# Kernel tuning notes

Measured on AMD Instinct MI355X. Metric: run time of the kernel, lower is better.

The kernel has to match this reference:

```python
import jax, jax.numpy as jnp
import numpy as np

GROUPS = 52
B, C, H, W = 16, 52, 256, 256  # c must equal groups (see t_value.view(b, c, 1, 1) in source)


def setup_inputs() -> dict:
    key = jax.random.key(0)
    ks = jax.random.split(key, 4)
    x = jax.random.normal(ks[0], (B, C, H, W), jnp.float32)
    weight = jax.random.normal(ks[1], (1, GROUPS, 1, 1), jnp.float32) * 0.1
    bias = jnp.ones((1, GROUPS, 1, 1), jnp.float32)
    one = jnp.ones((1, GROUPS, 1), jnp.float32)
    zero = jax.random.normal(ks[2], (1, GROUPS, 1), jnp.float32) * 0.1
    theta = jax.random.uniform(ks[3], (1, 2, 1, 1), jnp.float32)
    scale = jnp.ones((1,), jnp.float32)
    return dict(x=x, weight=weight, bias=bias, one=one, zero=zero, theta=theta, scale=scale)


def _prm_forward(x, weight, bias, one, zero, theta, scale):
    b, c, h, w = x.shape
    G = GROUPS
    cpg = c // G  # == 1 (required by original code)
    bg, hw = b * G, h * w

    xv = x.reshape(bg, cpg, hw)                      # [bg, cpg, hw]
    value = xv.sum(axis=1)                           # per-group channel-sum map [bg, hw]

    # adaptive max pool with indices (row-major argmax, first occurrence, same as torch)
    idx = jnp.argmax(value, axis=1)                  # [bg]
    qrow = (idx // w).astype(x.dtype)                # [bg]
    qcol = (idx % w).astype(x.dtype)                 # [bg]
    qval = jnp.take_along_axis(value, idx[:, None], axis=1)  # [bg, 1] == query_value

    # tiny per-group similarity matmuls (contraction over cpg)
    sim_max = jnp.einsum('gc,gch->gh', qval, xv)     # [bg, hw]
    gap = x.mean(axis=(2, 3)).reshape(bg, cpg)       # global avg pool per group-channel
    sim_gap = jnp.einsum('gc,gch->gh', gap, xv)      # [bg, hw]

    # positional Gaussian weighting: Normal(0, scale).log_prob(d * theta).exp()
    sigma = scale[0]
    log_norm = -jnp.log(sigma) - 0.5 * jnp.log(2.0 * jnp.pi)

    def gpdf(z):
        return jnp.exp(-0.5 * (z / sigma) ** 2 + log_norm)

    rows = jnp.arange(h, dtype=x.dtype)
    cols = jnp.arange(w, dtype=x.dtype)
    dr = jnp.abs(rows[None, :, None] - qrow[:, None, None])   # [bg, h, 1]
    dc = jnp.abs(cols[None, None, :] - qcol[:, None, None])   # [bg, 1, w]
    # mean over the 2 coordinate channels; broadcast avoids materializing [bg,2,h,w]
    dist = 0.5 * (gpdf(dr * theta[0, 0, 0, 0]) + gpdf(dc * theta[0, 1, 0, 0]))  # [bg, h, w]

    sim_max = sim_max.reshape(b, G, hw) * dist.reshape(b, G, hw)
    sim_gap = sim_gap.reshape(b, G, hw)
    sim = sim_max * zero + sim_gap * one             # [b, G, hw]

    # spatial mean/std normalization (torch .std -> ddof=1)
    ctx = sim - sim.mean(axis=2, keepdims=True)
    std = jnp.std(ctx, axis=2, keepdims=True, ddof=1) + 1e-05
    ctx = (ctx / std).reshape(b, G, h, w) * weight + bias

    # broadcast per-group gate over the group's channels, then sigmoid gate
    ctx = jnp.broadcast_to(ctx.reshape(bg, 1, h, w), (bg, cpg, h, w)).reshape(b, c, h, w)
    return x * jax.nn.sigmoid(ctx)


def reference(x, weight, bias, one, zero, theta, scale):
    return _prm_forward(x, weight, bias, one, zero, theta, scale)
```

## Files before the change

kernel.cpp:

```cpp
#include <hip/hip_runtime.h>
#include <math.h>

#define Gn 52
#define Hn 256
#define Wn 256
#define HW (Hn * Wn)
#define HW4 (HW / 4)
#define BG 832
#define TPB 1024
#define VPT 16

__global__ __launch_bounds__(TPB) void k_fused(
    const float4* __restrict__ x4,
    const float* __restrict__ weight, const float* __restrict__ bias,
    const float* __restrict__ one_,  const float* __restrict__ zero,
    const float* __restrict__ theta, const float* __restrict__ scale,
    float4* __restrict__ out4)
{
    const int bg   = blockIdx.x;
    const int g    = bg % Gn;
    const int t    = threadIdx.x;
    const int wave = t >> 6;
    const int lane = t & 63;
    const size_t base4 = (size_t)bg * HW4;
    const float4* xp = x4 + base4;

    float4 v[VPT];
    #pragma unroll
    for (int k = 0; k < VPT; ++k) v[k] = xp[t + k * TPB];

    float vmax = -INFINITY; int imax = 0; float sum = 0.f;
    #pragma unroll
    for (int k = 0; k < VPT; ++k) {
        int e = (t + k * TPB) * 4;
        float4 q = v[k];
        sum += (q.x + q.y) + (q.z + q.w);
        if (q.x > vmax) { vmax = q.x; imax = e; }
        if (q.y > vmax) { vmax = q.y; imax = e + 1; }
        if (q.z > vmax) { vmax = q.z; imax = e + 2; }
        if (q.w > vmax) { vmax = q.w; imax = e + 3; }
    }
    #pragma unroll
    for (int off = 32; off > 0; off >>= 1) {
        float ov = __shfl_down(vmax, off);
        int   oi = __shfl_down(imax, off);
        float os = __shfl_down(sum,  off);
        sum += os;
        if (ov > vmax || (ov == vmax && oi < imax)) { vmax = ov; imax = oi; }
    }
    __shared__ float rv[16];
    __shared__ int   ri[16];
    __shared__ float r1[16];
    __shared__ float r2[16];
    __shared__ float bc[6];
    if (lane == 0) { rv[wave] = vmax; ri[wave] = imax; r1[wave] = sum; }
    __syncthreads();
    if (t == 0) {
        float bv = rv[0]; int bi = ri[0]; float bs = r1[0];
        for (int i = 1; i < 16; ++i) {
            bs += r1[i];
            float ov = rv[i]; int oi = ri[i];
            if (ov > bv || (ov == bv && oi < bi)) { bv = ov; bi = oi; }
        }
        bc[0] = bv;
        bc[1] = (float)(bi >> 8);
        bc[2] = (float)(bi & 255);
        bc[3] = bs * (1.f / (float)HW);
    }
    __syncthreads();

    const float sigma   = scale[0];
    const float inv2s2  = 0.5f / (sigma * sigma);
    const float lognorm = -logf(sigma) - 0.9189385332046727f;
    const float th0 = theta[0], th1 = theta[1];
    const float qrow = bc[1], qcol = bc[2];
    const float A  = zero[g] * bc[0];
    const float Bc = one_[g] * bc[3];

    float s1 = 0.f, s2 = 0.f;
    #pragma unroll
    for (int k = 0; k < VPT; ++k) {
        int e = (t + k * TPB) * 4;
        float r = (float)(e >> 8);
        float c = (float)(e & 255);
        float zr = (r - qrow) * th0;
        float gr = __expf(lognorm - zr * zr * inv2s2);
        float4 q = v[k];
        #pragma unroll
        for (int j = 0; j < 4; ++j) {
            float vj = (j == 0) ? q.x : (j == 1) ? q.y : (j == 2) ? q.z : q.w;
            float zc = (c + (float)j - qcol) * th1;
            float gc = __expf(lognorm - zc * zc * inv2s2);
            float sim = (A * (0.5f * (gr + gc)) + Bc) * vj;
            s1 += sim;
            s2 += sim * sim;
        }
    }
    #pragma unroll
    for (int off = 32; off > 0; off >>= 1) {
        s1 += __shfl_down(s1, off);
        s2 += __shfl_down(s2, off);
    }
    if (lane == 0) { r1[wave] = s1; r2[wave] = s2; }
    __syncthreads();
    if (t == 0) {
        float S1 = 0.f, S2 = 0.f;
        for (int i = 0; i < 16; ++i) { S1 += r1[i]; S2 += r2[i]; }
        float mean = S1 * (1.f / (float)HW);
        float var  = (S2 - S1 * mean) * (1.f / (float)(HW - 1));
        var = fmaxf(var, 0.f);
        bc[4] = mean;
        bc[5] = weight[g] / (sqrtf(var) + 1e-5f);
    }
    __syncthreads();
    const float mean = bc[4], wsc = bc[5], bb = bias[g];

    #pragma unroll
    for (int k = 0; k < VPT; ++k) {
        int e = (t + k * TPB) * 4;
        float r = (float)(e >> 8);
        float c = (float)(e & 255);
        float zr = (r - qrow) * th0;
        float gr = __expf(lognorm - zr * zr * inv2s2);
        float4 q = v[k], o;
        #pragma unroll
        for (int j = 0; j < 4; ++j) {
            float vj = (j == 0) ? q.x : (j == 1) ? q.y : (j == 2) ? q.z : q.w;
            float zc = (c + (float)j - qcol) * th1;
            float gc = __expf(lognorm - zc * zc * inv2s2);
            float sim = (A * (0.5f * (gr + gc)) + Bc) * vj;
            float ctx = (sim - mean) * wsc + bb;
            float sg  = __builtin_amdgcn_rcpf(1.f + __expf(-ctx));
            float oj  = vj * sg;
            if (j == 0) o.x = oj; else if (j == 1) o.y = oj;
            else if (j == 2) o.z = oj; else o.w = oj;
        }
        out4[base4 + t + k * TPB] = o;
    }
}

extern "C" void kernel_launch(void* const* d_in, const int* in_sizes, int n_in,
                              void* d_out, int out_size, void* d_ws, size_t ws_size,
                              hipStream_t stream) {
    const float* x      = (const float*)d_in[0];
    const float* weight = (const float*)d_in[1];
    const float* bias   = (const float*)d_in[2];
    const float* one_   = (const float*)d_in[3];
    const float* zero   = (const float*)d_in[4];
    const float* theta  = (const float*)d_in[5];
    const float* scale  = (const float*)d_in[6];
    float* out = (float*)d_out;

    k_fused<<<BG, TPB, 0, stream>>>((const float4*)x, weight, bias, one_, zero,
                                    theta, scale, (float4*)out);
}
```

Baseline: 405.9 us.

## Precompute separable Gaussian row/column factors in LDS and streamline reductions

The per-element Gaussian weights are split into row and column terms. The 256 column values and 256 row values are computed once per block into shared memory, replacing two exp calls per element in each pass with one add. The final cross-wave reductions now use wave shuffles instead of a serial loop on thread 0. The argmax pass is split into two interleaved chains for more ILP, a launch-bounds occupancy hint is added, and the output uses nontemporal stores. The extra cost is more LDS use and one more barrier.

New measurement: 390.0 us. -3.9%, faster.

```diff
diff --git a/kernel.cpp b/kernel.cpp
--- a/kernel.cpp
+++ b/kernel.cpp
@@ -10,7 +10,9 @@
 #define TPB 1024
 #define VPT 16
 
-__global__ __launch_bounds__(TPB) void k_fused(
+typedef float vf4 __attribute__((ext_vector_type(4)));
+
+__global__ __launch_bounds__(TPB, 4) void k_fused(
     const float4* __restrict__ x4,
     const float* __restrict__ weight, const float* __restrict__ bias,
     const float* __restrict__ one_,  const float* __restrict__ zero,
@@ -25,21 +27,41 @@
     const size_t base4 = (size_t)bg * HW4;
     const float4* xp = x4 + base4;
 
+    __shared__ float rv[16];
+    __shared__ int   ri[16];
+    __shared__ float r1[16];
+    __shared__ float r2[16];
+    __shared__ float bc[6];
+    __shared__ float wcol[256];
+    __shared__ float urow[256];
+
     float4 v[VPT];
     #pragma unroll
     for (int k = 0; k < VPT; ++k) v[k] = xp[t + k * TPB];
 
-    float vmax = -INFINITY; int imax = 0; float sum = 0.f;
+    float vmaxA = -INFINITY, vmaxB = -INFINITY;
+    int   imaxA = 0x7fffffff, imaxB = 0x7fffffff;
+    float sumA = 0.f, sumB = 0.f;
     #pragma unroll
-    for (int k = 0; k < VPT; ++k) {
-        int e = (t + k * TPB) * 4;
-        float4 q = v[k];
-        sum += (q.x + q.y) + (q.z + q.w);
-        if (q.x > vmax) { vmax = q.x; imax = e; }
-        if (q.y > vmax) { vmax = q.y; imax = e + 1; }
-        if (q.z > vmax) { vmax = q.z; imax = e + 2; }
-        if (q.w > vmax) { vmax = q.w; imax = e + 3; }
+    for (int k = 0; k < VPT; k += 2) {
+        int e0 = (t + k * TPB) * 4;
+        float4 q0 = v[k];
+        sumA += (q0.x + q0.y) + (q0.z + q0.w);
+        if (q0.x > vmaxA) { vmaxA = q0.x; imaxA = e0; }
+        if (q0.y > vmaxA) { vmaxA = q0.y; imaxA = e0 + 1; }
+        if (q0.z > vmaxA) { vmaxA = q0.z; imaxA = e0 + 2; }
+        if (q0.w > vmaxA) { vmaxA = q0.w; imaxA = e0 + 3; }
+        int e1 = (t + (k + 1) * TPB) * 4;
+        float4 q1 = v[k + 1];
+        sumB += (q1.x + q1.y) + (q1.z + q1.w);
+        if (q1.x > vmaxB) { vmaxB = q1.x; imaxB = e1; }
+        if (q1.y > vmaxB) { vmaxB = q1.y; imaxB = e1 + 1; }
+        if (q1.z > vmaxB) { vmaxB = q1.z; imaxB = e1 + 2; }
+        if (q1.w > vmaxB) { vmaxB = q1.w; imaxB = e1 + 3; }
     }
+    float sum = sumA + sumB;
+    float vmax = vmaxA; int imax = imaxA;
+    if (vmaxB > vmax || (vmaxB == vmax && imaxB < imax)) { vmax = vmaxB; imax = imaxB; }
     #pragma unroll
     for (int off = 32; off > 0; off >>= 1) {
         float ov = __shfl_down(vmax, off);
@@ -48,53 +70,56 @@
         sum += os;
         if (ov > vmax || (ov == vmax && oi < imax)) { vmax = ov; imax = oi; }
     }
-    __shared__ float rv[16];
-    __shared__ int   ri[16];
-    __shared__ float r1[16];
-    __shared__ float r2[16];
-    __shared__ float bc[6];
     if (lane == 0) { rv[wave] = vmax; ri[wave] = imax; r1[wave] = sum; }
     __syncthreads();
-    if (t == 0) {
-        float bv = rv[0]; int bi = ri[0]; float bs = r1[0];
-        for (int i = 1; i < 16; ++i) {
-            bs += r1[i];
-            float ov = rv[i]; int oi = ri[i];
+    if (t < 64) {
+        float bv = (t < 16) ? rv[t] : -INFINITY;
+        int   bi = (t < 16) ? ri[t] : 0x7fffffff;
+        float bs = (t < 16) ? r1[t] : 0.f;
+        #pragma unroll
+        for (int off = 8; off > 0; off >>= 1) {
+            float ov = __shfl_down(bv, off);
+            int   oi = __shfl_down(bi, off);
+            float os = __shfl_down(bs, off);
+            bs += os;
             if (ov > bv || (ov == bv && oi < bi)) { bv = ov; bi = oi; }
         }
-        bc[0] = bv;
-        bc[1] = (float)(bi >> 8);
-        bc[2] = (float)(bi & 255);
-        bc[3] = bs * (1.f / (float)HW);
+        if (t == 0) {
+            bc[0] = bv;
+            bc[1] = (float)(bi >> 8);
+            bc[2] = (float)(bi & 255);
+            bc[3] = bs * (1.f / (float)HW);
+        }
     }
     __syncthreads();
 
     const float sigma   = scale[0];
     const float inv2s2  = 0.5f / (sigma * sigma);
     const float lognorm = -logf(sigma) - 0.9189385332046727f;
-    const float th0 = theta[0], th1 = theta[1];
-    const float qrow = bc[1], qcol = bc[2];
-    const float A  = zero[g] * bc[0];
-    const float Bc = one_[g] * bc[3];
+    const float A   = zero[g] * bc[0];
+    const float Bc  = one_[g] * bc[3];
+    const float A05 = 0.5f * A;
+    if (t < 256) {
+        float zc = ((float)t - bc[2]) * theta[1];
+        wcol[t] = A05 * __expf(lognorm - zc * zc * inv2s2);
+    } else if (t < 512) {
+        float zr = ((float)(t - 256) - bc[1]) * theta[0];
+        urow[t - 256] = A05 * __expf(lognorm - zr * zr * inv2s2) + Bc;
+    }
+    __syncthreads();
+
+    const float4 cw = *reinterpret_cast<const float4*>(&wcol[(t & 63) << 2]);
 
     float s1 = 0.f, s2 = 0.f;
     #pragma unroll
     for (int k = 0; k < VPT; ++k) {
-        int e = (t + k * TPB) * 4;
-        float r = (float)(e >> 8);
-        float c = (float)(e & 255);
-        float zr = (r - qrow) * th0;
-        float gr = __expf(lognorm - zr * zr * inv2s2);
+        const float ur = urow[wave + 16 * k];
         float4 q = v[k];
-        #pragma unroll
-        for (int j = 0; j < 4; ++j) {
-            float vj = (j == 0) ? q.x : (j == 1) ? q.y : (j == 2) ? q.z : q.w;
-            float zc = (c + (float)j - qcol) * th1;
-            float gc = __expf(lognorm - zc * zc * inv2s2);
-            float sim = (A * (0.5f * (gr + gc)) + Bc) * vj;
-            s1 += sim;
-            s2 += sim * sim;
-        }
+        float f, sim;
+        f = ur + cw.x; sim = f * q.x; s1 += sim; s2 = fmaf(sim, sim, s2);
+        f = ur + cw.y; sim = f * q.y; s1 += sim; s2 = fmaf(sim, sim, s2);
+        f = ur + cw.z; sim = f * q.z; s1 += sim; s2 = fmaf(sim, sim, s2);
+        f = ur + cw.w; sim = f * q.w; s1 += sim; s2 = fmaf(sim, sim, s2);
     }
     #pragma unroll
     for (int off = 32; off > 0; off >>= 1) {
@@ -103,39 +128,52 @@
     }
     if (lane == 0) { r1[wave] = s1; r2[wave] = s2; }
     __syncthreads();
-    if (t == 0) {
-        float S1 = 0.f, S2 = 0.f;
-        for (int i = 0; i < 16; ++i) { S1 += r1[i]; S2 += r2[i]; }
-        float mean = S1 * (1.f / (float)HW);
-        float var  = (S2 - S1 * mean) * (1.f / (float)(HW - 1));
-        var = fmaxf(var, 0.f);
-        bc[4] = mean;
-        bc[5] = weight[g] / (sqrtf(var) + 1e-5f);
+    if (t < 64) {
+        float S1 = (t < 16) ? r1[t] : 0.f;
+        float S2 = (t < 16) ? r2[t] : 0.f;
+        #pragma unroll
+        for (int off = 8; off > 0; off >>= 1) {
+            S1 += __shfl_down(S1, off);
+            S2 += __shfl_down(S2, off);
+        }
+        if (t == 0) {
+            float mean = S1 * (1.f / (float)HW);
+            float var  = (S2 - S1 * mean) * (1.f / (float)(HW - 1));
+            var = fmaxf(var, 0.f);
+            bc[4] = mean;
+            bc[5] = weight[g] / (sqrtf(var) + 1e-5f);
+        }
     }
     __syncthreads();
-    const float mean = bc[4], wsc = bc[5], bb = bias[g];
+    const float mean = bc[4], wsc = bc[5];
+    const float wb = fmaf(-mean, wsc, bias[g]);
 
     #pragma unroll
     for (int k = 0; k < VPT; ++k) {
-        int e = (t + k * TPB) * 4;
-        float r = (float)(e >> 8);
-        float c = (float)(e & 255);
-        float zr = (r - qrow) * th0;
-        float gr = __expf(lognorm - zr * zr * inv2s2);
-        float4 q = v[k], o;
-        #pragma unroll
-        for (int j = 0; j < 4; ++j) {
-            float vj = (j == 0) ? q.x : (j == 1) ? q.y : (j == 2) ? q.z : q.w;
-            float zc = (c + (float)j - qcol) * th1;
-            float gc = __expf(lognorm - zc * zc * inv2s2);
-            float sim = (A * (0.5f * (gr + gc)) + Bc) * vj;
-            float ctx = (sim - mean) * wsc + bb;
-            float sg  = __builtin_amdgcn_rcpf(1.f + __expf(-ctx));
-            float oj  = vj * sg;
-            if (j == 0) o.x = oj; else if (j == 1) o.y = oj;
-            else if (j == 2) o.z = oj; else o.w = oj;
+        const float ur = urow[wave + 16 * k];
+        float4 q = v[k];
+        vf4 o;
+        {
+            float f = ur + cw.x, sim = f * q.x;
+            float ctx = fmaf(sim, wsc, wb);
+            o.x = q.x * __builtin_amdgcn_rcpf(1.f + __expf(-ctx));
         }
-        out4[base4 + t + k * TPB] = o;
+        {
+            float f = ur + cw.y, sim = f * q.y;
+            float ctx = fmaf(sim, wsc, wb);
+            o.y = q.y * __builtin_amdgcn_rcpf(1.f + __expf(-ctx));
+        }
+        {
+            float f = ur + cw.z, sim = f * q.z;
+            float ctx = fmaf(sim, wsc, wb);
+            o.z = q.z * __builtin_amdgcn_rcpf(1.f + __expf(-ctx));
+        }
+        {
+            float f = ur + cw.w, sim = f * q.w;
+            float ctx = fmaf(sim, wsc, wb);
+            o.w = q.w * __builtin_amdgcn_rcpf(1.f + __expf(-ctx));
+        }
+        __builtin_nontemporal_store(o, reinterpret_cast<vf4*>(out4 + base4 + t + k * TPB));
     }
 }
 
```

## Split fused kernel into three strip-parallel passes with precomputed Gaussian tables

Applied to the files above, without the earlier changes.

Replaces the single kernel, which ran one 1024-thread block per slice and held the whole slice in registers, with three kernels that each split a slice into four strips of 256-thread blocks. Partial argmax, sum and moment statistics go through a small workspace buffer. Row and column Gaussian weights are precomputed into shared-memory tables, so the per-element exps drop to the sigmoid alone, and the output uses nontemporal stores. The aim is higher occupancy and less per-element transcendental work. In exchange x is read from global memory three times instead of once, and two extra launches are added.

New measurement: 434.3 us. 7.0% more time.

```diff
diff --git a/kernel.cpp b/kernel.cpp
--- a/kernel.cpp
+++ b/kernel.cpp
@@ -6,39 +6,41 @@
 #define Wn 256
 #define HW (Hn * Wn)
 #define HW4 (HW / 4)
-#define BG 832
-#define TPB 1024
-#define VPT 16
-
-__global__ __launch_bounds__(TPB) void k_fused(
-    const float4* __restrict__ x4,
-    const float* __restrict__ weight, const float* __restrict__ bias,
-    const float* __restrict__ one_,  const float* __restrict__ zero,
-    const float* __restrict__ theta, const float* __restrict__ scale,
-    float4* __restrict__ out4)
-{
-    const int bg   = blockIdx.x;
-    const int g    = bg % Gn;
-    const int t    = threadIdx.x;
-    const int wave = t >> 6;
-    const int lane = t & 63;
-    const size_t base4 = (size_t)bg * HW4;
-    const float4* xp = x4 + base4;
-
-    float4 v[VPT];
-    #pragma unroll
-    for (int k = 0; k < VPT; ++k) v[k] = xp[t + k * TPB];
-
-    float vmax = -INFINITY; int imax = 0; float sum = 0.f;
-    #pragma unroll
-    for (int k = 0; k < VPT; ++k) {
-        int e = (t + k * TPB) * 4;
-        float4 q = v[k];
-        sum += (q.x + q.y) + (q.z + q.w);
-        if (q.x > vmax) { vmax = q.x; imax = e; }
-        if (q.y > vmax) { vmax = q.y; imax = e + 1; }
-        if (q.z > vmax) { vmax = q.z; imax = e + 2; }
-        if (q.w > vmax) { vmax = q.w; imax = e + 3; }
+#define NSLICE 832
+#define SPB 4
+#define NBLK (NSLICE * SPB)
+#define TPB 256
+#define STRIP4 (HW4 / SPB)
+#define VPT (STRIP4 / TPB)
+#define WSS 24
+
+typedef float vf4 __attribute__((ext_vector_type(4)));
+
+__global__ __launch_bounds__(TPB) void k_p1(
+    const float4* __restrict__ x4, float* __restrict__ ws)
+{
+    const int blk = blockIdx.x;
+    const int bg = blk >> 2, q = blk & 3;
+    const int t = threadIdx.x;
+    const int wave = t >> 6, lane = t & 63;
+    const float4* xp = x4 + (size_t)bg * HW4 + q * STRIP4;
+
+    float vmax = -INFINITY; int imax = 0x7fffffff; float sum = 0.f;
+    #pragma unroll
+    for (int kk = 0; kk < VPT; kk += 4) {
+        float4 b[4];
+        #pragma unroll
+        for (int u = 0; u < 4; ++u) b[u] = xp[t + (kk + u) * TPB];
+        #pragma unroll
+        for (int u = 0; u < 4; ++u) {
+            int e = (q * STRIP4 + t + (kk + u) * TPB) * 4;
+            float4 v = b[u];
+            sum += (v.x + v.y) + (v.z + v.w);
+            if (v.x > vmax) { vmax = v.x; imax = e; }
+            if (v.y > vmax) { vmax = v.y; imax = e + 1; }
+            if (v.z > vmax) { vmax = v.z; imax = e + 2; }
+            if (v.w > vmax) { vmax = v.w; imax = e + 3; }
+        }
     }
     #pragma unroll
     for (int off = 32; off > 0; off >>= 1) {
@@ -48,52 +50,92 @@
         sum += os;
         if (ov > vmax || (ov == vmax && oi < imax)) { vmax = ov; imax = oi; }
     }
-    __shared__ float rv[16];
-    __shared__ int   ri[16];
-    __shared__ float r1[16];
-    __shared__ float r2[16];
-    __shared__ float bc[6];
-    if (lane == 0) { rv[wave] = vmax; ri[wave] = imax; r1[wave] = sum; }
+    __shared__ float rv[4]; __shared__ int ri[4]; __shared__ float rs[4];
+    if (lane == 0) { rv[wave] = vmax; ri[wave] = imax; rs[wave] = sum; }
     __syncthreads();
     if (t == 0) {
-        float bv = rv[0]; int bi = ri[0]; float bs = r1[0];
-        for (int i = 1; i < 16; ++i) {
-            bs += r1[i];
-            float ov = rv[i]; int oi = ri[i];
-            if (ov > bv || (ov == bv && oi < bi)) { bv = ov; bi = oi; }
-        }
-        bc[0] = bv;
-        bc[1] = (float)(bi >> 8);
-        bc[2] = (float)(bi & 255);
-        bc[3] = bs * (1.f / (float)HW);
-    }
-    __syncthreads();
+        float bv = rv[0]; int bi = ri[0]; float bs = rs[0];
+        #pragma unroll
+        for (int i = 1; i < 4; ++i) {
+            bs += rs[i];
+            if (rv[i] > bv || (rv[i] == bv && ri[i] < bi)) { bv = rv[i]; bi = ri[i]; }
+        }
+        float* w = ws + (size_t)bg * WSS;
+        w[q]     = bv;
+        w[4 + q] = (float)bi;
+        w[8 + q] = bs;
+    }
+}
+
+__device__ __forceinline__ void combine_amax(
+    const float* __restrict__ w, float& qrow, float& qcol, float& qval, float& gap)
+{
+    float bv = w[0], bif = w[4], bs = w[8];
+    #pragma unroll
+    for (int i = 1; i < 4; ++i) {
+        float vv = w[i], ii = w[4 + i];
+        if (vv > bv || (vv == bv && ii < bif)) { bv = vv; bif = ii; }
+        bs += w[8 + i];
+    }
+    int bi = (int)bif;
+    qrow = (float)(bi >> 8);
+    qcol = (float)(bi & 255);
+    qval = bv;
+    gap  = bs * (1.f / (float)HW);
+}
+
+__global__ __launch_bounds__(TPB) void k_p2(
+    const float4* __restrict__ x4, float* __restrict__ ws,
+    const float* __restrict__ one_, const float* __restrict__ zero,
+    const float* __restrict__ theta, const float* __restrict__ scale)
+{
+    const int blk = blockIdx.x;
+    const int bg = blk >> 2, q = blk & 3;
+    const int g = bg % Gn;
+    const int t = threadIdx.x;
+    const int wave = t >> 6, lane = t & 63;
+    const float4* xp = x4 + (size_t)bg * HW4 + q * STRIP4;
+    float* w = ws + (size_t)bg * WSS;
+
+    float qrow, qcol, qval, gap;
+    combine_amax(w, qrow, qcol, qval, gap);
 
     const float sigma   = scale[0];
     const float inv2s2  = 0.5f / (sigma * sigma);
     const float lognorm = -logf(sigma) - 0.9189385332046727f;
+    const float A05 = 0.5f * zero[g] * qval;
+    const float Bc  = one_[g] * gap;
     const float th0 = theta[0], th1 = theta[1];
-    const float qrow = bc[1], qcol = bc[2];
-    const float A  = zero[g] * bc[0];
-    const float Bc = one_[g] * bc[3];
+
+    __shared__ float wcol[256];
+    __shared__ float urow[64];
+    {
+        float zc = ((float)t - qcol) * th1;
+        wcol[t] = A05 * __expf(lognorm - zc * zc * inv2s2);
+        if (t < 64) {
+            float zr = ((float)(64 * q + t) - qrow) * th0;
+            urow[t] = A05 * __expf(lognorm - zr * zr * inv2s2) + Bc;
+        }
+    }
+    __syncthreads();
+
+    const float4 cw = *reinterpret_cast<const float4*>(&wcol[(4 * t) & 255]);
 
     float s1 = 0.f, s2 = 0.f;
     #pragma unroll
-    for (int k = 0; k < VPT; ++k) {
-        int e = (t + k * TPB) * 4;
-        float r = (float)(e >> 8);
-        float c = (float)(e & 255);
-        float zr = (r - qrow) * th0;
-        float gr = __expf(lognorm - zr * zr * inv2s2);
-        float4 q = v[k];
-        #pragma unroll
-        for (int j = 0; j < 4; ++j) {
-            float vj = (j == 0) ? q.x : (j == 1) ? q.y : (j == 2) ? q.z : q.w;
-            float zc = (c + (float)j - qcol) * th1;
-            float gc = __expf(lognorm - zc * zc * inv2s2);
-            float sim = (A * (0.5f * (gr + gc)) + Bc) * vj;
-            s1 += sim;
-            s2 += sim * sim;
+    for (int kk = 0; kk < VPT; kk += 4) {
+        float4 b[4];
+        #pragma unroll
+        for (int u = 0; u < 4; ++u) b[u] = xp[t + (kk + u) * TPB];
+        #pragma unroll
+        for (int u = 0; u < 4; ++u) {
+            const float ur = urow[4 * (kk + u) + (t >> 6)];
+            float4 v = b[u];
+            float f, sim;
+            f = ur + cw.x; sim = f * v.x; s1 += sim; s2 = fmaf(sim, sim, s2);
+            f = ur + cw.y; sim = f * v.y; s1 += sim; s2 = fmaf(sim, sim, s2);
+            f = ur + cw.z; sim = f * v.z; s1 += sim; s2 = fmaf(sim, sim, s2);
+            f = ur + cw.w; sim = f * v.w; s1 += sim; s2 = fmaf(sim, sim, s2);
         }
     }
     #pragma unroll
@@ -101,41 +143,86 @@
         s1 += __shfl_down(s1, off);
         s2 += __shfl_down(s2, off);
     }
+    __shared__ float r1[4], r2[4];
     if (lane == 0) { r1[wave] = s1; r2[wave] = s2; }
     __syncthreads();
     if (t == 0) {
-        float S1 = 0.f, S2 = 0.f;
-        for (int i = 0; i < 16; ++i) { S1 += r1[i]; S2 += r2[i]; }
-        float mean = S1 * (1.f / (float)HW);
-        float var  = (S2 - S1 * mean) * (1.f / (float)(HW - 1));
-        var = fmaxf(var, 0.f);
-        bc[4] = mean;
-        bc[5] = weight[g] / (sqrtf(var) + 1e-5f);
-    }
-    __syncthreads();
-    const float mean = bc[4], wsc = bc[5], bb = bias[g];
-
-    #pragma unroll
-    for (int k = 0; k < VPT; ++k) {
-        int e = (t + k * TPB) * 4;
-        float r = (float)(e >> 8);
-        float c = (float)(e & 255);
-        float zr = (r - qrow) * th0;
-        float gr = __expf(lognorm - zr * zr * inv2s2);
-        float4 q = v[k], o;
-        #pragma unroll
-        for (int j = 0; j < 4; ++j) {
-            float vj = (j == 0) ? q.x : (j == 1) ? q.y : (j == 2) ? q.z : q.w;
-            float zc = (c + (float)j - qcol) * th1;
-            float gc = __expf(lognorm - zc * zc * inv2s2);
-            float sim = (A * (0.5f * (gr + gc)) + Bc) * vj;
-            float ctx = (sim - mean) * wsc + bb;
-            float sg  = __builtin_amdgcn_rcpf(1.f + __expf(-ctx));
-            float oj  = vj * sg;
-            if (j == 0) o.x = oj; else if (j == 1) o.y = oj;
-            else if (j == 2) o.z = oj; else o.w = oj;
-        }
-        out4[base4 + t + k * TPB] = o;
+        float S1 = r1[0] + r1[1] + r1[2] + r1[3];
+        float S2 = r2[0] + r2[1] + r2[2] + r2[3];
+        w[12 + q] = S1;
+        w[16 + q] = S2;
+    }
+}
+
+__global__ __launch_bounds__(TPB) void k_p3(
+    const float4* __restrict__ x4, const float* __restrict__ ws,
+    const float* __restrict__ weight, const float* __restrict__ bias,
+    const float* __restrict__ one_, const float* __restrict__ zero,
+    const float* __restrict__ theta, const float* __restrict__ scale,
+    float4* __restrict__ out4)
+{
+    const int blk = blockIdx.x;
+    const int bg = blk >> 2, q = blk & 3;
+    const int g = bg % Gn;
+    const int t = threadIdx.x;
+    const size_t base4 = (size_t)bg * HW4 + q * STRIP4;
+    const float4* xp = x4 + base4;
+    const float* w = ws + (size_t)bg * WSS;
+
+    float qrow, qcol, qval, gap;
+    combine_amax(w, qrow, qcol, qval, gap);
+    const float S1 = (w[12] + w[13]) + (w[14] + w[15]);
+    const float S2 = (w[16] + w[17]) + (w[18] + w[19]);
+
+    const float sigma   = scale[0];
+    const float inv2s2  = 0.5f / (sigma * sigma);
+    const float lognorm = -logf(sigma) - 0.9189385332046727f;
+    const float A05 = 0.5f * zero[g] * qval;
+    const float Bc  = one_[g] * gap;
+    const float th0 = theta[0], th1 = theta[1];
+
+    const float mean = S1 * (1.f / (float)HW);
+    float var = (S2 - S1 * mean) * (1.f / (float)(HW - 1));
+    var = fmaxf(var, 0.f);
+    const float wsc = weight[g] / (sqrtf(var) + 1e-5f);
+    const float wb  = fmaf(-mean, wsc, bias[g]);
+
+    __shared__ float wcol[256];
+    __shared__ float urow[64];
+    {
+        float zc = ((float)t - qcol) * th1;
+        wcol[t] = A05 * __expf(lognorm - zc * zc * inv2s2);
+        if (t < 64) {
+            float zr = ((float)(64 * q + t) - qrow) * th0;
+            urow[t] = A05 * __expf(lognorm - zr * zr * inv2s2) + Bc;
+        }
+    }
+    __syncthreads();
+
+    const float4 cw = *reinterpret_cast<const float4*>(&wcol[(4 * t) & 255]);
+
+    #pragma unroll
+    for (int kk = 0; kk < VPT; kk += 4) {
+        float4 b[4];
+        #pragma unroll
+        for (int u = 0; u < 4; ++u) b[u] = xp[t + (kk + u) * TPB];
+        #pragma unroll
+        for (int u = 0; u < 4; ++u) {
+            const float ur = urow[4 * (kk + u) + (t >> 6)];
+            float4 v = b[u];
+            vf4 o;
+            float f, sim, ctx;
+            f = ur + cw.x; sim = f * v.x; ctx = fmaf(sim, wsc, wb);
+            o.x = v.x * __builtin_amdgcn_rcpf(1.f + __expf(-ctx));
+            f = ur + cw.y; sim = f * v.y; ctx = fmaf(sim, wsc, wb);
+            o.y = v.y * __builtin_amdgcn_rcpf(1.f + __expf(-ctx));
+            f = ur + cw.z; sim = f * v.z; ctx = fmaf(sim, wsc, wb);
+            o.z = v.z * __builtin_amdgcn_rcpf(1.f + __expf(-ctx));
+            f = ur + cw.w; sim = f * v.w; ctx = fmaf(sim, wsc, wb);
+            o.w = v.w * __builtin_amdgcn_rcpf(1.f + __expf(-ctx));
+            __builtin_nontemporal_store(o,
+                reinterpret_cast<vf4*>(out4 + base4 + t + (kk + u) * TPB));
+        }
     }
 }
 
@@ -150,7 +237,10 @@
     const float* theta  = (const float*)d_in[5];
     const float* scale  = (const float*)d_in[6];
     float* out = (float*)d_out;
-
-    k_fused<<<BG, TPB, 0, stream>>>((const float4*)x, weight, bias, one_, zero,
-                                    theta, scale, (float4*)out);
-}
+    float* ws  = (float*)d_ws;
+
+    k_p1<<<NBLK, TPB, 0, stream>>>((const float4*)x, ws);
+    k_p2<<<NBLK, TPB, 0, stream>>>((const float4*)x, ws, one_, zero, theta, scale);
+    k_p3<<<NBLK, TPB, 0, stream>>>((const float4*)x, ws, weight, bias, one_, zero,
+                                   theta, scale, (float4*)out);
+}
```
